# Optimization experiments

Measured on AMD Instinct MI355X. Metric: run time of the kernel, lower is better.

Reference implementation:

```python
import jax, jax.numpy as jnp
import numpy as np

N_HEAD = 12

def setup_inputs() -> dict:
    key = jax.random.key(0)
    k1, k2, k3 = jax.random.split(key, 3)
    B, T, C = 1, 4096, 768
    x = jax.random.normal(k1, (B, T, C), dtype=jnp.float32)
    w_attn = jax.random.normal(k2, (C, 3 * C), dtype=jnp.float32) * 0.02
    w_proj = jax.random.normal(k3, (C, C), dtype=jnp.float32) * 0.02
    return {"x": x, "w_attn": w_attn, "w_proj": w_proj}

def reference(x, w_attn, w_proj):
    B, T, C = x.shape
    H = N_HEAD
    hd = C // H
    scale = 1.0 / jnp.sqrt(jnp.asarray(hd, dtype=x.dtype))
    qkv = x @ w_attn  # [B,T,3C]
    q, k, v = jnp.split(qkv, 3, axis=-1)
    # [B,T,C] -> [B,H,T,hd]
    q = q.reshape(B, T, H, hd).transpose(0, 2, 1, 3)
    k = k.reshape(B, T, H, hd).transpose(0, 2, 1, 3)
    v = v.reshape(B, T, H, hd).transpose(0, 2, 1, 3)
    att = jnp.einsum("bhqd,bhkd->bhqk", q, k) * scale  # [B,H,T,T]
    causal = jnp.tril(jnp.ones((T, T), dtype=bool))
    att = jnp.where(causal[None, None], att, -jnp.inf)
    att = jax.nn.softmax(att, axis=-1)
    y = jnp.einsum("bhqk,bhkd->bhqd", att, v)  # [B,H,T,hd]
    y = y.transpose(0, 2, 1, 3).reshape(B, T, C)
    return y @ w_proj
```

## Files before the change

### kernel.cpp

```cpp
#include <hip/hip_runtime.h>
#include <hip/hip_bf16.h>

typedef __attribute__((ext_vector_type(8))) short bfx8;
typedef __attribute__((ext_vector_type(4))) short bfx4;
typedef __attribute__((ext_vector_type(4))) float f32x4;
typedef __attribute__((ext_vector_type(4))) unsigned int u32x4;
typedef __attribute__((ext_vector_type(2))) unsigned int u32x2;

#define T_SEQ 4096
#define C_DIM 768
#define NH    12
#define HD    64
#define QKV_N 2304
#define QK_N  1536

#define MFMA16(a, b, c) __builtin_amdgcn_mfma_f32_16x16x32_bf16((a), (b), (c), 0, 0, 0)

#if __has_builtin(__builtin_amdgcn_exp2f)
#define EXP2(x) __builtin_amdgcn_exp2f(x)
#else
#define EXP2(x) exp2f(x)
#endif

__device__ __forceinline__ short f2bf(float f) {
  __hip_bfloat16 h = __float2bfloat16(f);
  return __builtin_bit_cast(short, h);
}

__device__ __forceinline__ unsigned packtrunc(float p_even, float p_odd) {
#if __has_builtin(__builtin_amdgcn_perm)
  return __builtin_amdgcn_perm(__builtin_bit_cast(unsigned, p_odd),
                               __builtin_bit_cast(unsigned, p_even), 0x07060302u);
#else
  return (__builtin_bit_cast(unsigned, p_odd) & 0xFFFF0000u) |
         (__builtin_bit_cast(unsigned, p_even) >> 16);
#endif
}

__device__ __forceinline__ void pl16(unsigned& a, unsigned& b) {
#if __has_builtin(__builtin_amdgcn_permlane16_swap)
  u32x2 r = __builtin_amdgcn_permlane16_swap(a, b, false, false);
  a = r[0]; b = r[1];
#else
  unsigned ax = (unsigned)__shfl_xor((int)a, 16, 64);
  unsigned bx = (unsigned)__shfl_xor((int)b, 16, 64);
  bool odd = ((threadIdx.x >> 4) & 1) != 0;
  unsigned na = odd ? bx : a;
  unsigned nb = odd ? b : ax;
  a = na; b = nb;
#endif
}
__device__ __forceinline__ void pl32(unsigned& a, unsigned& b) {
#if __has_builtin(__builtin_amdgcn_permlane32_swap)
  u32x2 r = __builtin_amdgcn_permlane32_swap(a, b, false, false);
  a = r[0]; b = r[1];
#else
  unsigned ax = (unsigned)__shfl_xor((int)a, 32, 64);
  unsigned bx = (unsigned)__shfl_xor((int)b, 32, 64);
  bool hi = ((threadIdx.x >> 5) & 1) != 0;
  unsigned na = hi ? bx : a;
  unsigned nb = hi ? b : ax;
  a = na; b = nb;
#endif
}

#define NB_CONV 3072
#define NB_TA   (72 * 24)
#define NB_TB   (24 * 24)
__global__ __launch_bounds__(256) void prep_kernel(
    const float* __restrict__ x, short* __restrict__ xb,
    const float* __restrict__ w_attn, short* __restrict__ wab,
    const float* __restrict__ w_proj, short* __restrict__ wpb) {
  __shared__ short tile[32][33];
  const int b = blockIdx.x;
  if (b < NB_CONV) {
    int i = b * 256 + threadIdx.x;
    float4 v = ((const float4*)x)[i];
    bfx4 o;
    o[0] = f2bf(v.x); o[1] = f2bf(v.y); o[2] = f2bf(v.z); o[3] = f2bf(v.w);
    ((bfx4*)xb)[i] = o;
    return;
  }
  const float* in; short* out; int Cc, bx, by, qcols;
  if (b < NB_CONV + NB_TA) {
    int bb = b - NB_CONV;
    in = w_attn; out = wab; Cc = QKV_N;
    bx = (bb % 72) * 32; by = (bb / 72) * 32;
    qcols = C_DIM;
  } else {
    int bb = b - NB_CONV - NB_TA;
    in = w_proj; out = wpb; Cc = C_DIM;
    bx = (bb % 24) * 32; by = (bb / 24) * 32;
    qcols = 0;
  }
  int tx = threadIdx.x & 31, ty = threadIdx.x >> 5;
  float sc = (bx + tx) < qcols ? 0.125f * 1.4426950408889634f : 1.0f;
#pragma unroll
  for (int i = 0; i < 32; i += 8)
    tile[ty + i][tx] = f2bf(in[(size_t)(by + ty + i) * Cc + (bx + tx)] * sc);
  __syncthreads();
#pragma unroll
  for (int i = 0; i < 32; i += 8)
    out[(size_t)(bx + ty + i) * C_DIM + (by + tx)] = tile[tx][ty + i];
}

__global__ __launch_bounds__(256) void gemm_qkv(
    const short* __restrict__ A, const short* __restrict__ Bt,
    short* __restrict__ qk, short* __restrict__ Vt, int K) {
  __shared__ short As[2][128 * 32];
  __shared__ short Bs[2][128 * 32];
  const int tid  = threadIdx.x;
  const int lane = tid & 63;
  const int wave = tid >> 6;
  const int am0 = blockIdx.x * 128;
  const int bn0 = blockIdx.y * 96;
  const int wr = (wave >> 1) * 64;
  const int wc = (wave & 1) * 48;

  const int idx0 = tid,       r0 = idx0 >> 2, c0 = (idx0 & 3) * 8;
  const int idx1 = 256 + tid, r1 = idx1 >> 2, c1 = (idx1 & 3) * 8;
  const int rb0 = (r0 < 96) ? r0 : 95;
  const int rb1 = (r1 < 96) ? r1 : 95;

#define GSTAGE(buf, k0)                                                                 \
  do {                                                                                  \
    __builtin_amdgcn_global_load_lds(                                                   \
        (const __attribute__((address_space(1))) void*)(A + (size_t)(am0 + r0) * K + (k0) + c0), \
        (__attribute__((address_space(3))) void*)(&As[buf][idx0 * 8]), 16, 0, 0);       \
    __builtin_amdgcn_global_load_lds(                                                   \
        (const __attribute__((address_space(1))) void*)(A + (size_t)(am0 + r1) * K + (k0) + c1), \
        (__attribute__((address_space(3))) void*)(&As[buf][idx1 * 8]), 16, 0, 0);       \
    __builtin_amdgcn_global_load_lds(                                                   \
        (const __attribute__((address_space(1))) void*)(Bt + (size_t)(bn0 + rb0) * K + (k0) + c0), \
        (__attribute__((address_space(3))) void*)(&Bs[buf][idx0 * 8]), 16, 0, 0);       \
    __builtin_amdgcn_global_load_lds(                                                   \
        (const __attribute__((address_space(1))) void*)(Bt + (size_t)(bn0 + rb1) * K + (k0) + c1), \
        (__attribute__((address_space(3))) void*)(&Bs[buf][idx1 * 8]), 16, 0, 0);       \
  } while (0)

  const f32x4 zero = {0.f, 0.f, 0.f, 0.f};
  f32x4 acc[4][3];
#pragma unroll
  for (int i = 0; i < 4; i++)
#pragma unroll
    for (int j = 0; j < 3; j++) acc[i][j] = zero;

  const int aoff = (wr + (lane & 15)) * 32 + (lane >> 4) * 8;
  const int boff = (wc + (lane & 15)) * 32 + (lane >> 4) * 8;

  const int nk = K / 32;
  GSTAGE(0, 0);
  for (int t = 0; t < nk; t++) {
    const int cur = t & 1;
    if (t + 1 < nk) {
      GSTAGE(cur ^ 1, (t + 1) * 32);
      asm volatile("s_waitcnt vmcnt(4)" ::: "memory");
    } else {
      asm volatile("s_waitcnt vmcnt(0)" ::: "memory");
    }
    __builtin_amdgcn_s_barrier();

    bfx8 a[4], b[3];
#pragma unroll
    for (int mf = 0; mf < 4; mf++)
      a[mf] = *(const bfx8*)&As[cur][aoff + mf * 16 * 32];
#pragma unroll
    for (int nf = 0; nf < 3; nf++)
      b[nf] = *(const bfx8*)&Bs[cur][boff + nf * 16 * 32];
#pragma unroll
    for (int mf = 0; mf < 4; mf++)
#pragma unroll
      for (int nf = 0; nf < 3; nf++)
        acc[mf][nf] = MFMA16(a[mf], b[nf], acc[mf][nf]);

    asm volatile("s_waitcnt lgkmcnt(0)" ::: "memory");
    __builtin_amdgcn_s_barrier();
  }
#undef GSTAGE

  if (bn0 >= QK_N) {
#pragma unroll
    for (int mf = 0; mf < 4; mf++) {
      int row0 = am0 + wr + mf * 16 + (lane >> 4) * 4;
#pragma unroll
      for (int nf = 0; nf < 3; nf++) {
        int colV = bn0 - QK_N + wc + nf * 16 + (lane & 15);
        bfx4 ov;
#pragma unroll
        for (int r = 0; r < 4; r++) ov[r] = f2bf(acc[mf][nf][r]);
        *(bfx4*)&Vt[(size_t)colV * T_SEQ + row0] = ov;
      }
    }
  } else {
#pragma unroll
    for (int mf = 0; mf < 4; mf++) {
#pragma unroll
      for (int r = 0; r < 4; r++) {
        int row = am0 + wr + mf * 16 + (lane >> 4) * 4 + r;
#pragma unroll
        for (int nf = 0; nf < 3; nf++) {
          int col = bn0 + wc + nf * 16 + (lane & 15);
          qk[(size_t)row * QK_N + col] = f2bf(acc[mf][nf][r]);
        }
      }
    }
  }
}

__global__ __launch_bounds__(256) void gemm_proj(
    const short* __restrict__ A, const short* __restrict__ Bt,
    float* __restrict__ C, int N, int K) {
  __shared__ short As[2][64 * 32];
  __shared__ short Bs[2][64 * 32];
  const int tid  = threadIdx.x;
  const int lane = tid & 63;
  const int wave = tid >> 6;
  const int am0 = blockIdx.x * 64;
  const int bn0 = blockIdx.y * 64;
  const int wr = (wave >> 1) * 32;
  const int wc = (wave & 1) * 32;

  const int r0 = tid >> 2, c0 = (tid & 3) * 8;

#define PSTAGE(buf, k0)                                                                 \
  do {                                                                                  \
    __builtin_amdgcn_global_load_lds(                                                   \
        (const __attribute__((address_space(1))) void*)(A + (size_t)(am0 + r0) * K + (k0) + c0), \
        (__attribute__((address_space(3))) void*)(&As[buf][tid * 8]), 16, 0, 0);        \
    __builtin_amdgcn_global_load_lds(                                                   \
        (const __attribute__((address_space(1))) void*)(Bt + (size_t)(bn0 + r0) * K + (k0) + c0), \
        (__attribute__((address_space(3))) void*)(&Bs[buf][tid * 8]), 16, 0, 0);        \
  } while (0)

  const f32x4 zero = {0.f, 0.f, 0.f, 0.f};
  f32x4 acc[2][2];
#pragma unroll
  for (int i = 0; i < 2; i++)
#pragma unroll
    for (int j = 0; j < 2; j++) acc[i][j] = zero;

  const int aoff = (wr + (lane & 15)) * 32 + (lane >> 4) * 8;
  const int boff = (wc + (lane & 15)) * 32 + (lane >> 4) * 8;

  const int nk = K / 32;
  PSTAGE(0, 0);
  for (int t = 0; t < nk; t++) {
    const int cur = t & 1;
    if (t + 1 < nk) {
      PSTAGE(cur ^ 1, (t + 1) * 32);
      asm volatile("s_waitcnt vmcnt(2)" ::: "memory");
    } else {
      asm volatile("s_waitcnt vmcnt(0)" ::: "memory");
    }
    __builtin_amdgcn_s_barrier();

    bfx8 a[2], b[2];
#pragma unroll
    for (int mf = 0; mf < 2; mf++)
      a[mf] = *(const bfx8*)&As[cur][aoff + mf * 16 * 32];
#pragma unroll
    for (int nf = 0; nf < 2; nf++)
      b[nf] = *(const bfx8*)&Bs[cur][boff + nf * 16 * 32];
#pragma unroll
    for (int mf = 0; mf < 2; mf++)
#pragma unroll
      for (int nf = 0; nf < 2; nf++)
        acc[mf][nf] = MFMA16(a[mf], b[nf], acc[mf][nf]);

    asm volatile("s_waitcnt lgkmcnt(0)" ::: "memory");
    __builtin_amdgcn_s_barrier();
  }
#undef PSTAGE

#pragma unroll
  for (int mf = 0; mf < 2; mf++) {
#pragma unroll
    for (int r = 0; r < 4; r++) {
      int row = am0 + wr + mf * 16 + (lane >> 4) * 4 + r;
#pragma unroll
      for (int nf = 0; nf < 2; nf++) {
        int col = bn0 + wc + nf * 16 + (lane & 15);
        C[(size_t)row * N + col] = acc[mf][nf][r];
      }
    }
  }
}

__global__ __launch_bounds__(256) void attn_kernel(
    const short* __restrict__ qk, const short* __restrict__ Vt,
    short* __restrict__ yb) {
  __shared__ short Ks[3][64 * 64];
  __shared__ short Vs[3][64 * 64];

  const int tid  = threadIdx.x;
  const int lane = tid & 63;
  const int wv   = tid >> 6;
  const int col  = lane & 15;
  const int g    = lane >> 4;

  const int bid   = blockIdx.x;
  const int h     = bid % NH;
  const int q_idx = (T_SEQ / 64 - 1) - bid / NH;
  const int q0    = q_idx * 64;
  const int qw    = q0 + wv * 16;
  const int nt    = q_idx + 1;

  const int hq = h * HD;
  const int hk = C_DIM + h * HD;
  const short* Vth = Vt + (size_t)h * HD * T_SEQ;

  const int sidx0 = tid;
  const int sidx1 = 256 + tid;
  const int srow0 = sidx0 >> 3, sslot0 = (sidx0 & 7) ^ (srow0 & 7);
  const int srow1 = sidx1 >> 3, sslot1 = (sidx1 & 7) ^ (srow1 & 7);

#define STAGE(buf, kvoff)                                                               \
  do {                                                                                  \
    __builtin_amdgcn_global_load_lds(                                                   \
        (const __attribute__((address_space(1))) void*)(qk + (size_t)((kvoff) + srow0) * QK_N + hk + sslot0 * 8), \
        (__attribute__((address_space(3))) void*)(&Ks[buf][sidx0 * 8]), 16, 0, 0);      \
    __builtin_amdgcn_global_load_lds(                                                   \
        (const __attribute__((address_space(1))) void*)(qk + (size_t)((kvoff) + srow1) * QK_N + hk + sslot1 * 8), \
        (__attribute__((address_space(3))) void*)(&Ks[buf][sidx1 * 8]), 16, 0, 0);      \
    __builtin_amdgcn_global_load_lds(                                                   \
        (const __attribute__((address_space(1))) void*)(Vth + (size_t)srow0 * T_SEQ + (kvoff) + sslot0 * 8), \
        (__attribute__((address_space(3))) void*)(&Vs[buf][sidx0 * 8]), 16, 0, 0);      \
    __builtin_amdgcn_global_load_lds(                                                   \
        (const __attribute__((address_space(1))) void*)(Vth + (size_t)srow1 * T_SEQ + (kvoff) + sslot1 * 8), \
        (__attribute__((address_space(3))) void*)(&Vs[buf][sidx1 * 8]), 16, 0, 0);      \
  } while (0)

  bfx8 qf[2];
#pragma unroll
  for (int hf = 0; hf < 2; hf++)
    qf[hf] = *(const bfx8*)&qk[(size_t)(qw + col) * QK_N + hq + hf * 32 + g * 8];

  int koff[4][2], voff[2][4];
#pragma unroll
  for (int sub = 0; sub < 4; sub++) {
    int row = sub * 16 + col;
#pragma unroll
    for (int hf = 0; hf < 2; hf++)
      koff[sub][hf] = row * 64 + ((((hf << 2) | g) ^ (row & 7)) * 8);
  }
#pragma unroll
  for (int ks = 0; ks < 2; ks++)
#pragma unroll
    for (int c = 0; c < 4; c++) {
      int row = c * 16 + col;
      voff[ks][c] = row * 64 + ((((ks << 2) | g) ^ (row & 7)) * 8);
    }

  bfx8 ones;
#pragma unroll
  for (int j = 0; j < 8; j++) ones[j] = (short)0x3F80;

  const f32x4 zero = {0.f, 0.f, 0.f, 0.f};
  f32x4 o[4];
#pragma unroll
  for (int c = 0; c < 4; c++) o[c] = zero;
  f32x4 o_l = zero;

  const int qabs = qw + col;

#define TILE_BODY(BUF, KV)                                                              \
  do {                                                                                  \
    if ((KV) <= qw + 15) {                                                              \
      bfx8 kf[4][2];                                                                    \
      _Pragma("unroll") for (int sub = 0; sub < 4; sub++)                               \
          _Pragma("unroll") for (int hf = 0; hf < 2; hf++)                              \
              kf[sub][hf] = *(const bfx8*)&Ks[BUF][koff[sub][hf]];                      \
      bfx8 vtf[2][4];                                                                   \
      _Pragma("unroll") for (int ks = 0; ks < 2; ks++)                                  \
          _Pragma("unroll") for (int c = 0; c < 4; c++)                                 \
              vtf[ks][c] = *(const bfx8*)&Vs[BUF][voff[ks][c]];                         \
      f32x4 s[4];                                                                       \
      __builtin_amdgcn_s_setprio(1);                                                    \
      _Pragma("unroll") for (int sub = 0; sub < 4; sub++) {                             \
        s[sub] = zero;                                                                  \
        s[sub] = MFMA16(kf[sub][0], qf[0], s[sub]);                                     \
        s[sub] = MFMA16(kf[sub][1], qf[1], s[sub]);                                     \
      }                                                                                 \
      __builtin_amdgcn_s_setprio(0);                                                    \
      if (!((KV) + 63 <= qw)) {                                                         \
        _Pragma("unroll") for (int sub = 0; sub < 4; sub++)                             \
            _Pragma("unroll") for (int r = 0; r < 4; r++) {                             \
              int key = (KV) + sub * 16 + 4 * g + r;                                    \
              if (key > qabs) s[sub][r] = -INFINITY;                                    \
            }                                                                           \
      }                                                                                 \
      float p[4][4];                                                                    \
      _Pragma("unroll") for (int sub = 0; sub < 4; sub++)                               \
          _Pragma("unroll") for (int r = 0; r < 4; r++)                                 \
              p[sub][r] = EXP2(s[sub][r]);                                              \
      _Pragma("unroll") for (int ks = 0; ks < 2; ks++) {                                \
        unsigned x0 = packtrunc(p[2 * ks][0], p[2 * ks][1]);                            \
        unsigned y0 = packtrunc(p[2 * ks + 1][0], p[2 * ks + 1][1]);                    \
        unsigned x1 = packtrunc(p[2 * ks][2], p[2 * ks][3]);                            \
        unsigned y1 = packtrunc(p[2 * ks + 1][2], p[2 * ks + 1][3]);                    \
        pl32(x0, y0); pl16(x0, y0);                                                     \
        pl32(x1, y1); pl16(x1, y1);                                                     \
        u32x4 w; w[0] = x0; w[1] = x1; w[2] = y0; w[3] = y1;                            \
        bfx8 pf = __builtin_bit_cast(bfx8, w);                                          \
        __builtin_amdgcn_s_setprio(1);                                                  \
        _Pragma("unroll") for (int c = 0; c < 4; c++)                                   \
            o[c] = MFMA16(vtf[ks][c], pf, o[c]);                                        \
        o_l = MFMA16(ones, pf, o_l);                                                    \
        __builtin_amdgcn_s_setprio(0);                                                  \
      }                                                                                 \
    }                                                                                   \
  } while (0)

#define PHASE(BCUR, BNXT2)                                                              \
  do {                                                                                  \
    if (t + 1 < nt) { asm volatile("s_waitcnt vmcnt(4)" ::: "memory"); }                \
    else            { asm volatile("s_waitcnt vmcnt(0)" ::: "memory"); }                \
    __builtin_amdgcn_s_barrier();                                                       \
    if (t + 2 < nt) STAGE(BNXT2, (t + 2) * 64);                                         \
    TILE_BODY(BCUR, t * 64);                                                            \
    asm volatile("s_waitcnt lgkmcnt(0)" ::: "memory");                                  \
  } while (0)

  STAGE(0, 0);
  STAGE(1, 64);

  int t = 0;
  while (true) {
    PHASE(0, 2); if (++t >= nt) break;
    PHASE(1, 0); if (++t >= nt) break;
    PHASE(2, 1); if (++t >= nt) break;
  }

  float inv = 1.f / o_l[0];
#pragma unroll
  for (int c = 0; c < 4; c++) {
    bfx4 ov;
#pragma unroll
    for (int r = 0; r < 4; r++) ov[r] = f2bf(o[c][r] * inv);
    *(bfx4*)&yb[(size_t)(qw + col) * C_DIM + h * HD + c * 16 + g * 4] = ov;
  }
#undef PHASE
#undef TILE_BODY
#undef STAGE
}

extern "C" void kernel_launch(void* const* d_in, const int* in_sizes, int n_in,
                              void* d_out, int out_size, void* d_ws, size_t ws_size,
                              hipStream_t stream) {
  const float* x      = (const float*)d_in[0];
  const float* w_attn = (const float*)d_in[1];
  const float* w_proj = (const float*)d_in[2];
  float* out = (float*)d_out;

  char* ws = (char*)d_ws;
  short* xb  = (short*)(ws);
  short* wab = (short*)(ws + 6291456);
  short* wpb = (short*)(ws + 9830400);
  short* qk  = (short*)(ws + 11010048);
  short* Vt  = (short*)(ws + 23592960);
  short* yb  = (short*)(ws + 29884416);

  prep_kernel<<<NB_CONV + NB_TA + NB_TB, 256, 0, stream>>>(x, xb, w_attn, wab, w_proj, wpb);
  gemm_qkv<<<dim3(T_SEQ / 128, QKV_N / 96), 256, 0, stream>>>(xb, wab, qk, Vt, C_DIM);
  attn_kernel<<<(T_SEQ / 64) * NH, 256, 0, stream>>>(qk, Vt, yb);
  gemm_proj<<<dim3(T_SEQ / 64, C_DIM / 64), 256, 0, stream>>>(yb, wpb, out, C_DIM, C_DIM);
}
```

Measured before the change: 107.2 us.

## Split causal attention KV range across two blocks and merge in combine kernel

Each (head, query-tile) is now handled by two blocks that each process half of the causal KV tiles. They write unnormalized bf16 partial outputs and per-row sums, and a new combine kernel adds the partials and normalizes them. The goal is to double the number of blocks and shorten the longest causal block, so work is better balanced across CUs. In exchange there is an extra kernel launch, extra global traffic for the partials, and extra bf16 rounding of the unnormalized output. The K/V pipeline also drops from triple to double buffering and adds a second barrier per tile.

```diff
diff --git a/kernel.cpp b/kernel.cpp
--- a/kernel.cpp
+++ b/kernel.cpp
@@ -25,6 +25,10 @@
 __device__ __forceinline__ short f2bf(float f) {
   __hip_bfloat16 h = __float2bfloat16(f);
   return __builtin_bit_cast(short, h);
+}
+__device__ __forceinline__ float bf2f(short s) {
+  unsigned u = ((unsigned)(unsigned short)s) << 16;
+  return __builtin_bit_cast(float, u);
 }
 
 __device__ __forceinline__ unsigned packtrunc(float p_even, float p_odd) {
@@ -288,9 +292,9 @@
 
 __global__ __launch_bounds__(256) void attn_kernel(
     const short* __restrict__ qk, const short* __restrict__ Vt,
-    short* __restrict__ yb) {
-  __shared__ short Ks[3][64 * 64];
-  __shared__ short Vs[3][64 * 64];
+    short* __restrict__ p0, short* __restrict__ p1, float* __restrict__ lsums) {
+  __shared__ short Ks[2][64 * 64];
+  __shared__ short Vs[2][64 * 64];
 
   const int tid  = threadIdx.x;
   const int lane = tid & 63;
@@ -299,11 +303,17 @@
   const int g    = lane >> 4;
 
   const int bid   = blockIdx.x;
-  const int h     = bid % NH;
-  const int q_idx = (T_SEQ / 64 - 1) - bid / NH;
+  const int ch    = bid & 1;
+  const int pb    = bid >> 1;
+  const int h     = pb % NH;
+  const int q_idx = (T_SEQ / 64 - 1) - pb / NH;
   const int q0    = q_idx * 64;
   const int qw    = q0 + wv * 16;
   const int nt    = q_idx + 1;
+  const int half  = (nt + 1) >> 1;
+  const int t0    = ch ? half : 0;
+  const int t1    = ch ? nt : half;
+  short* pout     = ch ? p1 : p0;
 
   const int hq = h * HD;
   const int hk = C_DIM + h * HD;
@@ -411,37 +421,53 @@
     }                                                                                   \
   } while (0)
 
-#define PHASE(BCUR, BNXT2)                                                              \
-  do {                                                                                  \
-    if (t + 1 < nt) { asm volatile("s_waitcnt vmcnt(4)" ::: "memory"); }                \
-    else            { asm volatile("s_waitcnt vmcnt(0)" ::: "memory"); }                \
-    __builtin_amdgcn_s_barrier();                                                       \
-    if (t + 2 < nt) STAGE(BNXT2, (t + 2) * 64);                                         \
-    TILE_BODY(BCUR, t * 64);                                                            \
-    asm volatile("s_waitcnt lgkmcnt(0)" ::: "memory");                                  \
-  } while (0)
-
-  STAGE(0, 0);
-  STAGE(1, 64);
-
-  int t = 0;
-  while (true) {
-    PHASE(0, 2); if (++t >= nt) break;
-    PHASE(1, 0); if (++t >= nt) break;
-    PHASE(2, 1); if (++t >= nt) break;
-  }
-
-  float inv = 1.f / o_l[0];
+  if (t0 < t1) {
+    STAGE(0, t0 * 64);
+    for (int t = t0; t < t1; t++) {
+      const int cur = (t - t0) & 1;
+      if (t + 1 < t1) {
+        STAGE(cur ^ 1, (t + 1) * 64);
+        asm volatile("s_waitcnt vmcnt(4)" ::: "memory");
+      } else {
+        asm volatile("s_waitcnt vmcnt(0)" ::: "memory");
+      }
+      __builtin_amdgcn_s_barrier();
+      TILE_BODY(cur, t * 64);
+      asm volatile("s_waitcnt lgkmcnt(0)" ::: "memory");
+      __builtin_amdgcn_s_barrier();
+    }
+  }
+
+  if (g == 0)
+    lsums[(size_t)ch * NH * T_SEQ + (size_t)h * T_SEQ + qw + col] = o_l[0];
 #pragma unroll
   for (int c = 0; c < 4; c++) {
     bfx4 ov;
 #pragma unroll
-    for (int r = 0; r < 4; r++) ov[r] = f2bf(o[c][r] * inv);
-    *(bfx4*)&yb[(size_t)(qw + col) * C_DIM + h * HD + c * 16 + g * 4] = ov;
-  }
-#undef PHASE
+    for (int r = 0; r < 4; r++) ov[r] = f2bf(o[c][r]);
+    *(bfx4*)&pout[(size_t)(qw + col) * C_DIM + h * HD + c * 16 + g * 4] = ov;
+  }
 #undef TILE_BODY
 #undef STAGE
+}
+
+__global__ __launch_bounds__(256) void combine_kernel(
+    short* __restrict__ p0, const short* __restrict__ p1,
+    const float* __restrict__ lsums) {
+  int i = blockIdx.x * 256 + threadIdx.x;
+  int base = i * 8;
+  int q = base / C_DIM;
+  int h = (base % C_DIM) / HD;
+  float l = lsums[(size_t)h * T_SEQ + q] +
+            lsums[(size_t)NH * T_SEQ + (size_t)h * T_SEQ + q];
+  float inv = 1.f / l;
+  bfx8 a = *(const bfx8*)&p0[base];
+  bfx8 b = *(const bfx8*)&p1[base];
+  bfx8 y;
+#pragma unroll
+  for (int j = 0; j < 8; j++)
+    y[j] = f2bf((bf2f(a[j]) + bf2f(b[j])) * inv);
+  *(bfx8*)&p0[base] = y;
 }
 
 extern "C" void kernel_launch(void* const* d_in, const int* in_sizes, int n_in,
@@ -460,8 +486,12 @@
   short* Vt  = (short*)(ws + 23592960);
   short* yb  = (short*)(ws + 29884416);
 
+  short* p1    = xb;
+  float* lsums = (float*)wab;
+
   prep_kernel<<<NB_CONV + NB_TA + NB_TB, 256, 0, stream>>>(x, xb, w_attn, wab, w_proj, wpb);
   gemm_qkv<<<dim3(T_SEQ / 128, QKV_N / 96), 256, 0, stream>>>(xb, wab, qk, Vt, C_DIM);
-  attn_kernel<<<(T_SEQ / 64) * NH, 256, 0, stream>>>(qk, Vt, yb);
+  attn_kernel<<<(T_SEQ / 64) * NH * 2, 256, 0, stream>>>(qk, Vt, yb, p1, lsums);
+  combine_kernel<<<(T_SEQ * C_DIM / 8) / 256, 256, 0, stream>>>(yb, p1, lsums);
   gemm_proj<<<dim3(T_SEQ / 64, C_DIM / 64), 256, 0, stream>>>(yb, wpb, out, C_DIM, C_DIM);
 }
```

Result: faster. 100.3 us (median of 3 runs) (-6.4%).
